# Kernel tuning notes

Hardware: AMD Instinct MI355X
Metric: run time of the kernel (lower is better)

The kernel has to match this reference:

```python
import jax, jax.numpy as jnp
import numpy as np

B, L, C, H = 4, 1024, 768, 12
D = C // H  # head_ch = 64


def setup_inputs() -> dict:
    key = jax.random.key(0)
    ks = jax.random.split(key, 8)
    s = 1.0 / np.sqrt(C)
    return {
        "inputs_q": jax.random.normal(ks[0], (B, L, C), jnp.float32),
        "inputs_kv": jax.random.normal(ks[1], (B, L, C), jnp.float32),
        "Wq": jax.random.normal(ks[2], (C, H * D), jnp.float32) * s,
        "Wk": jax.random.normal(ks[3], (C, H * D), jnp.float32) * s,
        "Wv": jax.random.normal(ks[4], (C, H * D), jnp.float32) * s,
        "Wout": jax.random.normal(ks[5], (H * D, C), jnp.float32) * s,
        "W_pre": jax.random.normal(ks[6], (H, H), jnp.float32) * (1.0 / np.sqrt(H)),
        "W_post": jax.random.normal(ks[7], (H, H), jnp.float32) * (1.0 / np.sqrt(H)),
    }


def reference(inputs_q, inputs_kv, Wq, Wk, Wv, Wout, W_pre, W_post):
    # Linear projections (no bias), split into heads: b l (h d) -> b h l d
    def split_heads(x):
        b, l, _ = x.shape
        return x.reshape(b, l, H, D).transpose(0, 2, 1, 3)

    q = split_heads(inputs_q @ Wq) / jnp.sqrt(jnp.asarray(D, inputs_q.dtype))
    k = split_heads(inputs_kv @ Wk)
    v = split_heads(inputs_kv @ Wv)

    # Attention logits [b, h, l, k]
    weights = jnp.einsum('bhld,bhkd->bhlk', q, k)
    # Talking-heads: learned cross-head mixing pre-softmax
    weights = jnp.einsum('bhlk,hi->bilk', weights, W_pre)
    weights = jax.nn.softmax(weights, axis=-1)
    # Talking-heads post-softmax mixing
    weights = jnp.einsum('bhlk,hi->bilk', weights, W_post)

    scores = jnp.einsum('bhlk,bhkd->bhld', weights, v)
    scores = scores.transpose(0, 2, 1, 3).reshape(B, L, H * D)  # b l (h d)
    return scores @ Wout
```

## Files before the change

kernel.cpp:

```cpp
#include <hip/hip_runtime.h>
#include <hip/hip_bf16.h>

#define BB 4
#define LL 1024
#define CC 768
#define HH 12
#define DD 64

typedef unsigned short ushort_t;
typedef __attribute__((ext_vector_type(8))) short bf16x8;
typedef __attribute__((ext_vector_type(4))) float f32x4;
typedef __attribute__((ext_vector_type(2))) float f32x2;
typedef __attribute__((ext_vector_type(2))) unsigned u32x2;

__device__ inline ushort_t f2bf(float x) {
    union { float f; unsigned u; } v; v.f = x;
    unsigned r = (v.u + 0x7FFFu + ((v.u >> 16) & 1u)) >> 16;
    return (ushort_t)r;
}
__device__ inline float u2f(unsigned u) {
    union { unsigned u; float f; } v; v.u = u;
    return v.f;
}
__device__ inline unsigned pack2bf(float lo, float hi) {
    union { __hip_bfloat162 v; unsigned u; } r;
    r.v = __float22bfloat162_rn(make_float2(lo, hi));
    return r.u;
}

__device__ inline void stage_rows(const ushort_t* __restrict__ g, int stride,
                                  ushort_t* lds, int nbytes, int wave, int lane) {
    const int ko = (lane & 3) << 3;
    const int rsub = lane >> 2;
    for (int off = wave * 1024; off < nbytes; off += 4096) {
        int row = (off >> 6) + rsub;
        __builtin_amdgcn_global_load_lds(
            (const __attribute__((address_space(1))) void*)(g + (size_t)row * stride + ko),
            (__attribute__((address_space(3))) void*)(lds + (off >> 1)),
            16, 0, 0);
    }
}

__global__ __launch_bounds__(256) void prep(const float* __restrict__ q, const float* __restrict__ kv,
                                            const float* __restrict__ w0, const float* __restrict__ w1,
                                            const float* __restrict__ w2, const float* __restrict__ w3,
                                            ushort_t* __restrict__ qo, ushort_t* __restrict__ kvo,
                                            ushort_t* __restrict__ o0, ushort_t* __restrict__ o1,
                                            ushort_t* __restrict__ o2, ushort_t* __restrict__ o3,
                                            float* __restrict__ Zp) {
    __shared__ float t[32][33];
    const int bx = blockIdx.x;
    if (bx < 3072) {
        const float* src = bx < 1536 ? q : kv;
        ushort_t* dst = bx < 1536 ? qo : kvo;
        int bb = bx < 1536 ? bx : bx - 1536;
        size_t i = ((size_t)bb * 256 + threadIdx.x) * 8;
        float4 a = *(const float4*)(src + i);
        float4 b = *(const float4*)(src + i + 4);
        ushort_t u[8] = {f2bf(a.x), f2bf(a.y), f2bf(a.z), f2bf(a.w),
                         f2bf(b.x), f2bf(b.y), f2bf(b.z), f2bf(b.w)};
        *(uint4*)(dst + i) = *(uint4*)u;
    } else if (bx < 5376) {
        int w = bx - 3072;
        int z = w / 576, rem = w % 576;
        const float* W = z == 0 ? w0 : z == 1 ? w1 : z == 2 ? w2 : w3;
        ushort_t* Wt   = z == 0 ? o0 : z == 1 ? o1 : z == 2 ? o2 : o3;
        const int c = threadIdx.x & 31, r0 = threadIdx.x >> 5;
        const int kb = (rem / 24) * 32, nb = (rem % 24) * 32;
#pragma unroll
        for (int i = 0; i < 4; ++i)
            t[r0 + 8 * i][c] = W[(size_t)(kb + r0 + 8 * i) * CC + nb + c];
        __syncthreads();
#pragma unroll
        for (int i = 0; i < 4; ++i)
            Wt[(size_t)(nb + r0 + 8 * i) * CC + kb + c] = f2bf(t[c][r0 + 8 * i]);
    } else {
        Zp[(bx - 5376) * 256 + threadIdx.x] = 0.f;
    }
}

__global__ __launch_bounds__(256) void proj_gemm(const ushort_t* __restrict__ Aq,
                                                 const ushort_t* __restrict__ Akv,
                                                 const ushort_t* __restrict__ Wqt,
                                                 const ushort_t* __restrict__ Wkt,
                                                 const ushort_t* __restrict__ Wvt,
                                                 ushort_t* __restrict__ Qo,
                                                 ushort_t* __restrict__ Ko,
                                                 ushort_t* __restrict__ Vto) {
    const int z = blockIdx.z;
    const ushort_t* A  = (z == 0) ? Aq : Akv;
    const ushort_t* Wt = (z == 0) ? Wqt : (z == 1 ? Wkt : Wvt);

    __shared__ __align__(16) ushort_t a_lds[128 * 32];
    __shared__ __align__(16) ushort_t b_lds[128 * 32];

    const int tid = threadIdx.x;
    const int bm = blockIdx.x * 128, bn = blockIdx.y * 128;
    const int wave = tid >> 6, lane = tid & 63;
    const int quad = lane >> 4, lq = lane & 15;
    const int wr = wave >> 1, wc = wave & 1;

    f32x4 acc[4][4] = {};

    for (int k0 = 0; k0 < CC; k0 += 32) {
        stage_rows(A + (size_t)bm * CC + k0, CC, a_lds, 8192, wave, lane);
        stage_rows(Wt + (size_t)bn * CC + k0, CC, b_lds, 8192, wave, lane);
        __syncthreads();
        bf16x8 af[4], bfr[4];
#pragma unroll
        for (int mi = 0; mi < 4; ++mi)
            af[mi] = *(bf16x8*)&a_lds[(wr * 64 + mi * 16 + lq) * 32 + quad * 8];
#pragma unroll
        for (int ni = 0; ni < 4; ++ni)
            bfr[ni] = *(bf16x8*)&b_lds[(wc * 64 + ni * 16 + lq) * 32 + quad * 8];
#pragma unroll
        for (int mi = 0; mi < 4; ++mi)
#pragma unroll
            for (int ni = 0; ni < 4; ++ni)
                acc[mi][ni] = __builtin_amdgcn_mfma_f32_16x16x32_bf16(af[mi], bfr[ni], acc[mi][ni], 0, 0, 0);
        __syncthreads();
    }

    const float scale = (z == 0) ? 0.125f : 1.0f;
#pragma unroll
    for (int mi = 0; mi < 4; ++mi)
#pragma unroll
        for (int ni = 0; ni < 4; ++ni)
#pragma unroll
            for (int r = 0; r < 4; ++r) {
                int row = bm + wr * 64 + mi * 16 + quad * 4 + r;
                int col = bn + wc * 64 + ni * 16 + lq;
                int b = row >> 10, l = row & 1023, h = col >> 6, d = col & 63;
                ushort_t v = f2bf(acc[mi][ni][r] * scale);
                if (z == 2) {
                    Vto[((size_t)(b * HH + h) * DD + d) * LL + l] = v;
                } else {
                    size_t off = (size_t)(b * HH + h) * (LL * DD)
                               + (size_t)(((l >> 4) * 8 + (d >> 3)) * 128 + (l & 15) * 8 + (d & 7));
                    if (z == 0) Qo[off] = v;
                    else        Ko[off] = v;
                }
            }
}

__global__ __launch_bounds__(256) void qk_premix(const ushort_t* __restrict__ Qf,
                                                 const ushort_t* __restrict__ Kf,
                                                 const float* __restrict__ Wpre,
                                                 ushort_t* __restrict__ E,
                                                 float* __restrict__ Z) {
    const int tid = threadIdx.x;
    const int lane = tid & 63, wave = tid >> 6;
    const int quad = lane >> 4, lq = lane & 15;
    const int wr = wave >> 1, wc = wave & 1;

    const int x = blockIdx.x;
    const int xcd = x & 7;
    const int b = xcd >> 1;
    const int s = x >> 3;
    const int bk = (s & 31) << 5;
    const int bl = ((((s >> 5) << 1) | (xcd & 1))) << 5;

    const ushort_t* Kp = Kf + (size_t)b * HH * LL * DD
                       + (size_t)(((bk >> 4) + wr) * 1024 + quad * 128 + lq * 8);
    const ushort_t* Qp = Qf + (size_t)b * HH * LL * DD
                       + (size_t)(((bl >> 4) + wc) * 1024 + quad * 128 + lq * 8);

    f32x4 acc[HH] = {};
#pragma unroll
    for (int h = 0; h < HH; ++h) {
        const size_t ho = (size_t)h * (LL * DD);
        bf16x8 ka0 = *(const bf16x8*)(Kp + ho);
        bf16x8 ka1 = *(const bf16x8*)(Kp + ho + 512);
        bf16x8 qb0 = *(const bf16x8*)(Qp + ho);
        bf16x8 qb1 = *(const bf16x8*)(Qp + ho + 512);
        acc[h] = __builtin_amdgcn_mfma_f32_16x16x32_bf16(ka0, qb0, acc[h], 0, 0, 0);
        acc[h] = __builtin_amdgcn_mfma_f32_16x16x32_bf16(ka1, qb1, acc[h], 0, 0, 0);
    }

    unsigned pk[6][4];
#pragma unroll
    for (int i2 = 0; i2 < 6; ++i2) {
        f32x4 m0 = {}, m1 = {};
#pragma unroll
        for (int h = 0; h < HH; ++h) {
            m0 += acc[h] * Wpre[h * HH + 2 * i2];
            m1 += acc[h] * Wpre[h * HH + 2 * i2 + 1];
        }
#pragma unroll
        for (int r = 0; r < 4; ++r)
            pk[i2][r] = pack2bf(__expf(m0[r]), __expf(m1[r]));
    }

    float zp[HH];
#pragma unroll
    for (int i2 = 0; i2 < 6; ++i2) {
        float s0 = 0.f, s1 = 0.f;
#pragma unroll
        for (int r = 0; r < 4; ++r) {
            s0 += u2f(pk[i2][r] << 16);
            s1 += u2f(pk[i2][r] & 0xFFFF0000u);
        }
        zp[2 * i2] = s0; zp[2 * i2 + 1] = s1;
    }
#pragma unroll
    for (int i = 0; i < HH; ++i) {
        zp[i] += __shfl_xor(zp[i], 16);
        zp[i] += __shfl_xor(zp[i], 32);
    }
    if (quad == 0) {
#pragma unroll
        for (int i = 0; i < HH; ++i)
            atomicAdd(&Z[((size_t)b * HH + i) * LL + bl + wc * 16 + lq], zp[i]);
    }

#pragma unroll
    for (int r = 0; r < 4; ++r) {
        ushort_t* ep = E + (((size_t)b * LL + bk + wr * 16 + quad * 4 + r) * LL
                            + bl + wc * 16 + lq) * HH;
        u32x2 s0; s0.x = pk[0][r]; s0.y = pk[1][r];
        u32x2 s1; s1.x = pk[2][r]; s1.y = pk[3][r];
        u32x2 s2; s2.x = pk[4][r]; s2.y = pk[5][r];
        __builtin_nontemporal_store(s0, (u32x2*)ep);
        __builtin_nontemporal_store(s1, (u32x2*)(ep + 4));
        __builtin_nontemporal_store(s2, (u32x2*)(ep + 8));
    }
}

__global__ __launch_bounds__(512) void pv_postmix(const ushort_t* __restrict__ E,
                                                  const ushort_t* __restrict__ Vt,
                                                  const float* __restrict__ Wpost,
                                                  const float* __restrict__ Z,
                                                  ushort_t* __restrict__ att) {
    __shared__ __align__(16) ushort_t p_lds[2][HH * 16 * 64];

    const int tid = threadIdx.x;
    const int lane = tid & 63, wave = tid >> 6;
    const int quad = lane >> 4, lq = lane & 15;
    const int ig = (wave >> 2) * 6;
    const int wd = wave & 3;
    const int lmix = tid & 15, kp = tid >> 4;

    const int bid = blockIdx.x;
    const int xcd = bid & 7;
    const int b = xcd >> 1;
    const int bl = ((((bid >> 3) << 1) | (xcd & 1))) << 4;

    float invZ[HH];
#pragma unroll
    for (int h = 0; h < HH; ++h)
        invZ[h] = 1.0f / Z[((size_t)b * HH + h) * LL + bl + lmix];

    const size_t vrow = ((size_t)(b * HH) * DD + wd * 16 + lq) * LL;
    const ushort_t* ebase = E + (((size_t)b * LL + kp * 2) * LL + bl + lmix) * HH;
    const size_t estep = (size_t)LL * HH;

    f32x4 acc[6] = {};
    u32x2 er[6];

#pragma unroll
    for (int j = 0; j < 3; ++j) {
        er[j]     = __builtin_nontemporal_load((const u32x2*)(ebase + 4 * j));
        er[j + 3] = __builtin_nontemporal_load((const u32x2*)(ebase + estep + 4 * j));
    }

#pragma unroll 1
    for (int kt = 0; kt < 16; ++kt) {
        unsigned w0[6] = {er[0].x, er[0].y, er[1].x, er[1].y, er[2].x, er[2].y};
        unsigned w1[6] = {er[3].x, er[3].y, er[4].x, er[4].y, er[5].x, er[5].y};
        f32x2 m[HH] = {};
#pragma unroll
        for (int h2 = 0; h2 < 6; ++h2) {
            f32x2 pe, po;
            pe.x = u2f(w0[h2] << 16);           pe.y = u2f(w1[h2] << 16);
            po.x = u2f(w0[h2] & 0xFFFF0000u);   po.y = u2f(w1[h2] & 0xFFFF0000u);
            pe *= invZ[2 * h2];
            po *= invZ[2 * h2 + 1];
#pragma unroll
            for (int i = 0; i < HH; ++i) {
                m[i] += pe * Wpost[(2 * h2) * HH + i];
                m[i] += po * Wpost[(2 * h2 + 1) * HH + i];
            }
        }

        if (kt < 15) {
            const ushort_t* ep = ebase + (size_t)(kt + 1) * 64 * estep;
#pragma unroll
            for (int j = 0; j < 3; ++j) {
                er[j]     = __builtin_nontemporal_load((const u32x2*)(ep + 4 * j));
                er[j + 3] = __builtin_nontemporal_load((const u32x2*)(ep + estep + 4 * j));
            }
        }

        {
            const int cs = (kp >> 2) ^ (lmix & 7);
            unsigned* pw = (unsigned*)p_lds[kt & 1];
#pragma unroll
            for (int i = 0; i < HH; ++i)
                pw[(i * 16 + lmix) * 32 + cs * 4 + (kp & 3)] = pack2bf(m[i].x, m[i].y);
        }

        asm volatile("s_waitcnt lgkmcnt(0)" ::: "memory");
        __builtin_amdgcn_s_barrier();
        asm volatile("" ::: "memory");

        const ushort_t* pb = p_lds[kt & 1];
#pragma unroll
        for (int k0 = 0; k0 < 2; ++k0)
#pragma unroll
            for (int ii = 0; ii < 6; ++ii) {
                const int hh = ig + ii;
                const int chl = (k0 << 2) + quad;
                const int chs = chl ^ (lq & 7);
                bf16x8 pa  = *(bf16x8*)&pb[(hh * 16 + lq) * 64 + chs * 8];
                bf16x8 vbf = *(const bf16x8*)(Vt + vrow + (size_t)hh * (DD * LL)
                                              + kt * 64 + chl * 8);
                acc[ii] = __builtin_amdgcn_mfma_f32_16x16x32_bf16(pa, vbf, acc[ii], 0, 0, 0);
            }
    }

#pragma unroll
    for (int ii = 0; ii < 6; ++ii)
#pragma unroll
        for (int r = 0; r < 4; ++r)
            att[((size_t)b * LL + bl + quad * 4 + r) * CC + (ig + ii) * 64 + wd * 16 + lq] =
                f2bf(acc[ii][r]);
}

__global__ __launch_bounds__(256) void out_gemm(const ushort_t* __restrict__ A,
                                                const ushort_t* __restrict__ Wt,
                                                float* __restrict__ out) {
    __shared__ __align__(16) ushort_t a_lds[128 * 32];
    __shared__ __align__(16) ushort_t b_lds[64 * 32];

    const int tid = threadIdx.x;
    const int bm = blockIdx.x * 128, bn = blockIdx.y * 64;
    const int wave = tid >> 6, lane = tid & 63;
    const int quad = lane >> 4, lq = lane & 15;
    const int wr = wave >> 1, wc = wave & 1;

    f32x4 acc[4][2] = {};

    for (int k0 = 0; k0 < CC; k0 += 32) {
        stage_rows(A + (size_t)bm * CC + k0, CC, a_lds, 8192, wave, lane);
        stage_rows(Wt + (size_t)bn * CC + k0, CC, b_lds, 4096, wave, lane);
        __syncthreads();
        bf16x8 af[4], bfr[2];
#pragma unroll
        for (int mi = 0; mi < 4; ++mi)
            af[mi] = *(bf16x8*)&a_lds[(wr * 64 + mi * 16 + lq) * 32 + quad * 8];
#pragma unroll
        for (int ni = 0; ni < 2; ++ni)
            bfr[ni] = *(bf16x8*)&b_lds[(wc * 32 + ni * 16 + lq) * 32 + quad * 8];
#pragma unroll
        for (int mi = 0; mi < 4; ++mi)
#pragma unroll
            for (int ni = 0; ni < 2; ++ni)
                acc[mi][ni] = __builtin_amdgcn_mfma_f32_16x16x32_bf16(af[mi], bfr[ni], acc[mi][ni], 0, 0, 0);
        __syncthreads();
    }

#pragma unroll
    for (int mi = 0; mi < 4; ++mi)
#pragma unroll
        for (int ni = 0; ni < 2; ++ni)
#pragma unroll
            for (int r = 0; r < 4; ++r) {
                int row = bm + wr * 64 + mi * 16 + quad * 4 + r;
                int col = bn + wc * 32 + ni * 16 + lq;
                out[(size_t)row * CC + col] = acc[mi][ni][r];
            }
}

extern "C" void kernel_launch(void* const* d_in, const int* in_sizes, int n_in,
                              void* d_out, int out_size, void* d_ws, size_t ws_size,
                              hipStream_t stream) {
    const float* inputs_q  = (const float*)d_in[0];
    const float* inputs_kv = (const float*)d_in[1];
    const float* Wq   = (const float*)d_in[2];
    const float* Wk   = (const float*)d_in[3];
    const float* Wv   = (const float*)d_in[4];
    const float* Wout = (const float*)d_in[5];
    const float* Wpre  = (const float*)d_in[6];
    const float* Wpost = (const float*)d_in[7];
    float* out = (float*)d_out;

    const size_t nS   = (size_t)BB * HH * LL * LL;
    const size_t nQKV = (size_t)BB * HH * LL * DD;
    const size_t nW   = (size_t)CC * CC;

    ushort_t* Eb   = (ushort_t*)d_ws;
    ushort_t* Qb   = Eb + nS;
    ushort_t* Kb   = Qb + nQKV;
    ushort_t* Vtb  = Kb + nQKV;
    ushort_t* attb = Vtb + nQKV;
    ushort_t* inq  = attb + nQKV;
    ushort_t* inkv = inq + nQKV;
    ushort_t* Wqt  = inkv + nQKV;
    ushort_t* Wkt  = Wqt + nW;
    ushort_t* Wvt  = Wkt + nW;
    ushort_t* Wot  = Wvt + nW;
    float*    Zb   = (float*)(Wot + nW);

    dim3 blk(256);

    prep<<<dim3(5568), blk, 0, stream>>>(inputs_q, inputs_kv, Wq, Wk, Wv, Wout,
                                         inq, inkv, Wqt, Wkt, Wvt, Wot, Zb);
    proj_gemm<<<dim3(32, 6, 3), blk, 0, stream>>>(inq, inkv, Wqt, Wkt, Wvt, Qb, Kb, Vtb);
    qk_premix<<<dim3(4096), blk, 0, stream>>>(Qb, Kb, Wpre, Eb, Zb);
    pv_postmix<<<dim3(256), dim3(512), 0, stream>>>(Eb, Vtb, Wpost, Zb, attb);
    out_gemm<<<dim3(32, 12), blk, 0, stream>>>(attb, Wot, out);
}
```

Baseline: 265.3 us.

## Split pv_postmix across head groups into 512 smaller blocks

The post-mix/PV kernel now launches 512 blocks of 256 threads, each handling one group of 6 output heads, instead of 256 blocks of 512 threads covering all 12 heads. Each thread post-mixes 4 key rows for only its 6 heads, which halves the LDS buffer and raises block count and occupancy. In exchange, the E tensor is read twice (once per head group) and the nontemporal loads become regular loads. V fragments are also batched into registers before the MFMA loop.

```diff
diff --git a/kernel.cpp b/kernel.cpp
--- a/kernel.cpp
+++ b/kernel.cpp
@@ -226,77 +226,93 @@
     }
 }
 
-__global__ __launch_bounds__(512) void pv_postmix(const ushort_t* __restrict__ E,
-                                                  const ushort_t* __restrict__ Vt,
-                                                  const float* __restrict__ Wpost,
-                                                  const float* __restrict__ Z,
-                                                  ushort_t* __restrict__ att) {
-    __shared__ __align__(16) ushort_t p_lds[2][HH * 16 * 64];
+__global__ __launch_bounds__(256, 3) void pv_postmix(const ushort_t* __restrict__ E,
+                                                     const ushort_t* __restrict__ Vt,
+                                                     const float* __restrict__ Wpost,
+                                                     const float* __restrict__ Z,
+                                                     ushort_t* __restrict__ att) {
+    __shared__ __align__(16) ushort_t p_lds[2][6 * 16 * 64];
 
     const int tid = threadIdx.x;
     const int lane = tid & 63, wave = tid >> 6;
     const int quad = lane >> 4, lq = lane & 15;
-    const int ig = (wave >> 2) * 6;
-    const int wd = wave & 3;
+    const int wd = wave;
     const int lmix = tid & 15, kp = tid >> 4;
 
     const int bid = blockIdx.x;
     const int xcd = bid & 7;
     const int b = xcd >> 1;
-    const int bl = ((((bid >> 3) << 1) | (xcd & 1))) << 4;
+    const int s = bid >> 3;
+    const int hg = s >> 5;
+    const int ig = hg * 6;
+    const int bl = ((((s & 31) << 1) | (xcd & 1))) << 4;
 
     float invZ[HH];
 #pragma unroll
     for (int h = 0; h < HH; ++h)
         invZ[h] = 1.0f / Z[((size_t)b * HH + h) * LL + bl + lmix];
 
-    const size_t vrow = ((size_t)(b * HH) * DD + wd * 16 + lq) * LL;
-    const ushort_t* ebase = E + (((size_t)b * LL + kp * 2) * LL + bl + lmix) * HH;
     const size_t estep = (size_t)LL * HH;
+    const ushort_t* ebase = E + (((size_t)b * LL + kp * 4) * LL + bl + lmix) * HH;
+    const size_t vbase = ((size_t)(b * HH + ig) * DD + wd * 16 + lq) * LL;
 
     f32x4 acc[6] = {};
-    u32x2 er[6];
-
-#pragma unroll
-    for (int j = 0; j < 3; ++j) {
-        er[j]     = __builtin_nontemporal_load((const u32x2*)(ebase + 4 * j));
-        er[j + 3] = __builtin_nontemporal_load((const u32x2*)(ebase + estep + 4 * j));
-    }
+    u32x2 er[12];
+
+#pragma unroll
+    for (int u = 0; u < 2; ++u)
+#pragma unroll
+        for (int j = 0; j < 3; ++j) {
+            er[u * 6 + j]     = *(const u32x2*)(ebase + (size_t)(2 * u) * estep + 4 * j);
+            er[u * 6 + 3 + j] = *(const u32x2*)(ebase + (size_t)(2 * u + 1) * estep + 4 * j);
+        }
 
 #pragma unroll 1
     for (int kt = 0; kt < 16; ++kt) {
-        unsigned w0[6] = {er[0].x, er[0].y, er[1].x, er[1].y, er[2].x, er[2].y};
-        unsigned w1[6] = {er[3].x, er[3].y, er[4].x, er[4].y, er[5].x, er[5].y};
-        f32x2 m[HH] = {};
-#pragma unroll
-        for (int h2 = 0; h2 < 6; ++h2) {
-            f32x2 pe, po;
-            pe.x = u2f(w0[h2] << 16);           pe.y = u2f(w1[h2] << 16);
-            po.x = u2f(w0[h2] & 0xFFFF0000u);   po.y = u2f(w1[h2] & 0xFFFF0000u);
-            pe *= invZ[2 * h2];
-            po *= invZ[2 * h2 + 1];
-#pragma unroll
-            for (int i = 0; i < HH; ++i) {
-                m[i] += pe * Wpost[(2 * h2) * HH + i];
-                m[i] += po * Wpost[(2 * h2 + 1) * HH + i];
+        unsigned pkw[2][6];
+#pragma unroll
+        for (int u = 0; u < 2; ++u) {
+            unsigned w0[6] = {er[u*6+0].x, er[u*6+0].y, er[u*6+1].x, er[u*6+1].y, er[u*6+2].x, er[u*6+2].y};
+            unsigned w1[6] = {er[u*6+3].x, er[u*6+3].y, er[u*6+4].x, er[u*6+4].y, er[u*6+5].x, er[u*6+5].y};
+            f32x2 m[6] = {};
+#pragma unroll
+            for (int h2 = 0; h2 < 6; ++h2) {
+                f32x2 pe, po;
+                pe.x = u2f(w0[h2] << 16);           pe.y = u2f(w1[h2] << 16);
+                po.x = u2f(w0[h2] & 0xFFFF0000u);   po.y = u2f(w1[h2] & 0xFFFF0000u);
+                pe *= invZ[2 * h2];
+                po *= invZ[2 * h2 + 1];
+#pragma unroll
+                for (int i = 0; i < 6; ++i) {
+                    m[i] += pe * Wpost[(2 * h2) * HH + ig + i];
+                    m[i] += po * Wpost[(2 * h2 + 1) * HH + ig + i];
+                }
             }
+#pragma unroll
+            for (int i = 0; i < 6; ++i) pkw[u][i] = pack2bf(m[i].x, m[i].y);
         }
 
         if (kt < 15) {
             const ushort_t* ep = ebase + (size_t)(kt + 1) * 64 * estep;
 #pragma unroll
-            for (int j = 0; j < 3; ++j) {
-                er[j]     = __builtin_nontemporal_load((const u32x2*)(ep + 4 * j));
-                er[j + 3] = __builtin_nontemporal_load((const u32x2*)(ep + estep + 4 * j));
+            for (int u = 0; u < 2; ++u)
+#pragma unroll
+                for (int j = 0; j < 3; ++j) {
+                    er[u * 6 + j]     = *(const u32x2*)(ep + (size_t)(2 * u) * estep + 4 * j);
+                    er[u * 6 + 3 + j] = *(const u32x2*)(ep + (size_t)(2 * u + 1) * estep + 4 * j);
+                }
+        }
+
+        {
+            unsigned* pw = (unsigned*)p_lds[kt & 1];
+#pragma unroll
+            for (int u = 0; u < 2; ++u) {
+                const int w = kp * 2 + u;
+                const int word = (((w >> 2) ^ (lmix & 7)) << 2) + (w & 3);
+#pragma unroll
+                for (int i = 0; i < 6; ++i)
+                    pw[(i * 16 + lmix) * 32 + word] = pkw[u][i];
             }
-        }
-
-        {
-            const int cs = (kp >> 2) ^ (lmix & 7);
-            unsigned* pw = (unsigned*)p_lds[kt & 1];
-#pragma unroll
-            for (int i = 0; i < HH; ++i)
-                pw[(i * 16 + lmix) * 32 + cs * 4 + (kp & 3)] = pack2bf(m[i].x, m[i].y);
         }
 
         asm volatile("s_waitcnt lgkmcnt(0)" ::: "memory");
@@ -305,17 +321,19 @@
 
         const ushort_t* pb = p_lds[kt & 1];
 #pragma unroll
-        for (int k0 = 0; k0 < 2; ++k0)
+        for (int k0 = 0; k0 < 2; ++k0) {
+            bf16x8 vf[6];
+#pragma unroll
+            for (int ii = 0; ii < 6; ++ii)
+                vf[ii] = *(const bf16x8*)(Vt + vbase + (size_t)ii * (DD * LL)
+                                          + kt * 64 + k0 * 32 + quad * 8);
+            const int chs = ((k0 << 2) + quad) ^ (lq & 7);
 #pragma unroll
             for (int ii = 0; ii < 6; ++ii) {
-                const int hh = ig + ii;
-                const int chl = (k0 << 2) + quad;
-                const int chs = chl ^ (lq & 7);
-                bf16x8 pa  = *(bf16x8*)&pb[(hh * 16 + lq) * 64 + chs * 8];
-                bf16x8 vbf = *(const bf16x8*)(Vt + vrow + (size_t)hh * (DD * LL)
-                                              + kt * 64 + chl * 8);
-                acc[ii] = __builtin_amdgcn_mfma_f32_16x16x32_bf16(pa, vbf, acc[ii], 0, 0, 0);
+                bf16x8 pa = *(bf16x8*)&pb[(ii * 16 + lq) * 64 + chs * 8];
+                acc[ii] = __builtin_amdgcn_mfma_f32_16x16x32_bf16(pa, vf[ii], acc[ii], 0, 0, 0);
             }
+        }
     }
 
 #pragma unroll
@@ -407,6 +425,6 @@
                                          inq, inkv, Wqt, Wkt, Wvt, Wot, Zb);
     proj_gemm<<<dim3(32, 6, 3), blk, 0, stream>>>(inq, inkv, Wqt, Wkt, Wvt, Qb, Kb, Vtb);
     qk_premix<<<dim3(4096), blk, 0, stream>>>(Qb, Kb, Wpre, Eb, Zb);
-    pv_postmix<<<dim3(256), dim3(512), 0, stream>>>(Eb, Vtb, Wpost, Zb, attb);
+    pv_postmix<<<dim3(512), blk, 0, stream>>>(Eb, Vtb, Wpost, Zb, attb);
     out_gemm<<<dim3(32, 12), blk, 0, stream>>>(attb, Wot, out);
 }
```

Measured after the change: 264.6 us. Within noise of the previous version (-0.3%).

## Tile E layout per query tile and build post-mix MFMA operands in registers

Applied to the files above, without the earlier changes.

The qk_premix kernel now writes the exp-logit tensor E in a layout blocked by 16-query tile, so each pv_postmix block reads one contiguous slice. pv_postmix drops its LDS staging and barrier. Each wave now computes the post-softmax head mixing for its own 3 output heads directly in registers, packing the results straight into MFMA A-operands, and double-buffers E loads in registers. The work per block moves from 512 to 256 threads, which means each wave recomputes the normalisation per head group, and register pressure rises considerably.

```diff
diff --git a/kernel.cpp b/kernel.cpp
--- a/kernel.cpp
+++ b/kernel.cpp
@@ -213,10 +213,11 @@
             atomicAdd(&Z[((size_t)b * HH + i) * LL + bl + wc * 16 + lq], zp[i]);
     }
 
+    const int ltw = (bl >> 4) + wc;
 #pragma unroll
     for (int r = 0; r < 4; ++r) {
-        ushort_t* ep = E + (((size_t)b * LL + bk + wr * 16 + quad * 4 + r) * LL
-                            + bl + wc * 16 + lq) * HH;
+        const int k = bk + wr * 16 + quad * 4 + r;
+        ushort_t* ep = E + (((size_t)(b * 64 + ltw) * 1024 + k) * 16 + lq) * 12;
         u32x2 s0; s0.x = pk[0][r]; s0.y = pk[1][r];
         u32x2 s1; s1.x = pk[2][r]; s1.y = pk[3][r];
         u32x2 s2; s2.x = pk[4][r]; s2.y = pk[5][r];
@@ -226,104 +227,122 @@
     }
 }
 
-__global__ __launch_bounds__(512) void pv_postmix(const ushort_t* __restrict__ E,
-                                                  const ushort_t* __restrict__ Vt,
-                                                  const float* __restrict__ Wpost,
-                                                  const float* __restrict__ Z,
-                                                  ushort_t* __restrict__ att) {
-    __shared__ __align__(16) ushort_t p_lds[2][HH * 16 * 64];
-
+__global__ __launch_bounds__(256, 1) void pv_postmix(const ushort_t* __restrict__ E,
+                                                     const ushort_t* __restrict__ Vt,
+                                                     const float* __restrict__ Wpost,
+                                                     const float* __restrict__ Z,
+                                                     ushort_t* __restrict__ att) {
     const int tid = threadIdx.x;
     const int lane = tid & 63, wave = tid >> 6;
     const int quad = lane >> 4, lq = lane & 15;
-    const int ig = (wave >> 2) * 6;
-    const int wd = wave & 3;
-    const int lmix = tid & 15, kp = tid >> 4;
+    const int hh0 = wave * 3;
 
     const int bid = blockIdx.x;
     const int xcd = bid & 7;
     const int b = xcd >> 1;
-    const int bl = ((((bid >> 3) << 1) | (xcd & 1))) << 4;
+    const int lt = ((bid >> 3) << 1) | (xcd & 1);
+    const int bl = lt << 4;
+
+    float wp[HH][3];
+#pragma unroll
+    for (int h = 0; h < HH; ++h)
+#pragma unroll
+        for (int ii = 0; ii < 3; ++ii)
+            wp[h][ii] = Wpost[h * HH + hh0 + ii];
 
     float invZ[HH];
 #pragma unroll
     for (int h = 0; h < HH; ++h)
-        invZ[h] = 1.0f / Z[((size_t)b * HH + h) * LL + bl + lmix];
-
-    const size_t vrow = ((size_t)(b * HH) * DD + wd * 16 + lq) * LL;
-    const ushort_t* ebase = E + (((size_t)b * LL + kp * 2) * LL + bl + lmix) * HH;
-    const size_t estep = (size_t)LL * HH;
-
-    f32x4 acc[6] = {};
-    u32x2 er[6];
-
-#pragma unroll
-    for (int j = 0; j < 3; ++j) {
-        er[j]     = __builtin_nontemporal_load((const u32x2*)(ebase + 4 * j));
-        er[j + 3] = __builtin_nontemporal_load((const u32x2*)(ebase + estep + 4 * j));
-    }
-
+        invZ[h] = 1.0f / Z[((size_t)b * HH + h) * LL + bl + lq];
+
+    const ushort_t* eslice = E + (size_t)(b * 64 + lt) * (1024 * 192)
+                           + (size_t)(quad * 8) * 192 + lq * 12;
+    const ushort_t* vbase = Vt + ((size_t)(b * HH + hh0) * DD + lq) * LL + quad * 8;
+
+    f32x4 acc[3][4] = {};
+    u32x2 eA[24], eB[24];
+    bf16x8 vf[12];
+
+#define LOADE(dst, kt_, k0_)                                                              \
+    do {                                                                                  \
+        const ushort_t* ep_ = eslice + (size_t)((kt_) * 64 + (k0_) * 32) * 192;           \
+        _Pragma("unroll")                                                                 \
+        for (int j_ = 0; j_ < 8; ++j_)                                                    \
+            _Pragma("unroll")                                                             \
+            for (int c_ = 0; c_ < 3; ++c_)                                                \
+                dst[j_ * 3 + c_] = *(const u32x2*)(ep_ + j_ * 192 + c_ * 4);              \
+    } while (0)
+
+#define LOADV(kt_, k0_)                                                                   \
+    do {                                                                                  \
+        _Pragma("unroll")                                                                 \
+        for (int ii_ = 0; ii_ < 3; ++ii_)                                                 \
+            _Pragma("unroll")                                                             \
+            for (int dq_ = 0; dq_ < 4; ++dq_)                                             \
+                vf[ii_ * 4 + dq_] = *(const bf16x8*)(vbase                                \
+                    + (size_t)(ii_ * DD + dq_ * 16) * LL + (kt_) * 64 + (k0_) * 32);      \
+    } while (0)
+
+#define HALF(src)                                                                         \
+    do {                                                                                  \
+        union { bf16x8 v; unsigned d[4]; } pa_[3];                                        \
+        _Pragma("unroll")                                                                 \
+        for (int j2_ = 0; j2_ < 4; ++j2_) {                                               \
+            float p0_[3] = {0.f, 0.f, 0.f}, p1_[3] = {0.f, 0.f, 0.f};                     \
+            _Pragma("unroll")                                                             \
+            for (int c_ = 0; c_ < 3; ++c_) {                                              \
+                u32x2 ea_ = src[(2 * j2_) * 3 + c_];                                      \
+                u32x2 eb_ = src[(2 * j2_ + 1) * 3 + c_];                                  \
+                float f0_ = u2f(ea_.x << 16)         * invZ[4 * c_ + 0];                  \
+                float f1_ = u2f(ea_.x & 0xFFFF0000u) * invZ[4 * c_ + 1];                  \
+                float f2_ = u2f(ea_.y << 16)         * invZ[4 * c_ + 2];                  \
+                float f3_ = u2f(ea_.y & 0xFFFF0000u) * invZ[4 * c_ + 3];                  \
+                float g0_ = u2f(eb_.x << 16)         * invZ[4 * c_ + 0];                  \
+                float g1_ = u2f(eb_.x & 0xFFFF0000u) * invZ[4 * c_ + 1];                  \
+                float g2_ = u2f(eb_.y << 16)         * invZ[4 * c_ + 2];                  \
+                float g3_ = u2f(eb_.y & 0xFFFF0000u) * invZ[4 * c_ + 3];                  \
+                _Pragma("unroll")                                                         \
+                for (int ii_ = 0; ii_ < 3; ++ii_) {                                       \
+                    p0_[ii_] += f0_ * wp[4 * c_ + 0][ii_] + f1_ * wp[4 * c_ + 1][ii_]     \
+                              + f2_ * wp[4 * c_ + 2][ii_] + f3_ * wp[4 * c_ + 3][ii_];    \
+                    p1_[ii_] += g0_ * wp[4 * c_ + 0][ii_] + g1_ * wp[4 * c_ + 1][ii_]     \
+                              + g2_ * wp[4 * c_ + 2][ii_] + g3_ * wp[4 * c_ + 3][ii_];    \
+                }                                                                         \
+            }                                                                             \
+            _Pragma("unroll")                                                             \
+            for (int ii_ = 0; ii_ < 3; ++ii_)                                             \
+                pa_[ii_].d[j2_] = pack2bf(p0_[ii_], p1_[ii_]);                            \
+        }                                                                                 \
+        _Pragma("unroll")                                                                 \
+        for (int ii_ = 0; ii_ < 3; ++ii_)                                                 \
+            _Pragma("unroll")                                                             \
+            for (int dq_ = 0; dq_ < 4; ++dq_)                                             \
+                acc[ii_][dq_] = __builtin_amdgcn_mfma_f32_16x16x32_bf16(                  \
+                    pa_[ii_].v, vf[ii_ * 4 + dq_], acc[ii_][dq_], 0, 0, 0);               \
+    } while (0)
+
+    LOADE(eA, 0, 0);
 #pragma unroll 1
     for (int kt = 0; kt < 16; ++kt) {
-        unsigned w0[6] = {er[0].x, er[0].y, er[1].x, er[1].y, er[2].x, er[2].y};
-        unsigned w1[6] = {er[3].x, er[3].y, er[4].x, er[4].y, er[5].x, er[5].y};
-        f32x2 m[HH] = {};
-#pragma unroll
-        for (int h2 = 0; h2 < 6; ++h2) {
-            f32x2 pe, po;
-            pe.x = u2f(w0[h2] << 16);           pe.y = u2f(w1[h2] << 16);
-            po.x = u2f(w0[h2] & 0xFFFF0000u);   po.y = u2f(w1[h2] & 0xFFFF0000u);
-            pe *= invZ[2 * h2];
-            po *= invZ[2 * h2 + 1];
-#pragma unroll
-            for (int i = 0; i < HH; ++i) {
-                m[i] += pe * Wpost[(2 * h2) * HH + i];
-                m[i] += po * Wpost[(2 * h2 + 1) * HH + i];
-            }
-        }
-
-        if (kt < 15) {
-            const ushort_t* ep = ebase + (size_t)(kt + 1) * 64 * estep;
-#pragma unroll
-            for (int j = 0; j < 3; ++j) {
-                er[j]     = __builtin_nontemporal_load((const u32x2*)(ep + 4 * j));
-                er[j + 3] = __builtin_nontemporal_load((const u32x2*)(ep + estep + 4 * j));
-            }
-        }
-
-        {
-            const int cs = (kp >> 2) ^ (lmix & 7);
-            unsigned* pw = (unsigned*)p_lds[kt & 1];
-#pragma unroll
-            for (int i = 0; i < HH; ++i)
-                pw[(i * 16 + lmix) * 32 + cs * 4 + (kp & 3)] = pack2bf(m[i].x, m[i].y);
-        }
-
-        asm volatile("s_waitcnt lgkmcnt(0)" ::: "memory");
-        __builtin_amdgcn_s_barrier();
-        asm volatile("" ::: "memory");
-
-        const ushort_t* pb = p_lds[kt & 1];
-#pragma unroll
-        for (int k0 = 0; k0 < 2; ++k0)
-#pragma unroll
-            for (int ii = 0; ii < 6; ++ii) {
-                const int hh = ig + ii;
-                const int chl = (k0 << 2) + quad;
-                const int chs = chl ^ (lq & 7);
-                bf16x8 pa  = *(bf16x8*)&pb[(hh * 16 + lq) * 64 + chs * 8];
-                bf16x8 vbf = *(const bf16x8*)(Vt + vrow + (size_t)hh * (DD * LL)
-                                              + kt * 64 + chl * 8);
-                acc[ii] = __builtin_amdgcn_mfma_f32_16x16x32_bf16(pa, vbf, acc[ii], 0, 0, 0);
-            }
-    }
-
-#pragma unroll
-    for (int ii = 0; ii < 6; ++ii)
-#pragma unroll
-        for (int r = 0; r < 4; ++r)
-            att[((size_t)b * LL + bl + quad * 4 + r) * CC + (ig + ii) * 64 + wd * 16 + lq] =
-                f2bf(acc[ii][r]);
+        LOADE(eB, kt, 1);
+        LOADV(kt, 0);
+        HALF(eA);
+        if (kt < 15) LOADE(eA, kt + 1, 0);
+        LOADV(kt, 1);
+        HALF(eB);
+    }
+#undef LOADE
+#undef LOADV
+#undef HALF
+
+#pragma unroll
+    for (int ii = 0; ii < 3; ++ii)
+#pragma unroll
+        for (int dq = 0; dq < 4; ++dq)
+#pragma unroll
+            for (int r = 0; r < 4; ++r)
+                att[((size_t)b * LL + bl + quad * 4 + r) * CC + (hh0 + ii) * 64 + dq * 16 + lq] =
+                    f2bf(acc[ii][dq][r]);
 }
 
 __global__ __launch_bounds__(256) void out_gemm(const ushort_t* __restrict__ A,
@@ -407,6 +426,6 @@
                                          inq, inkv, Wqt, Wkt, Wvt, Wot, Zb);
     proj_gemm<<<dim3(32, 6, 3), blk, 0, stream>>>(inq, inkv, Wqt, Wkt, Wvt, Qb, Kb, Vtb);
     qk_premix<<<dim3(4096), blk, 0, stream>>>(Qb, Kb, Wpre, Eb, Zb);
-    pv_postmix<<<dim3(256), dim3(512), 0, stream>>>(Eb, Vtb, Wpost, Zb, attb);
+    pv_postmix<<<dim3(256), blk, 0, stream>>>(Eb, Vtb, Wpost, Zb, attb);
     out_gemm<<<dim3(32, 12), blk, 0, stream>>>(attb, Wot, out);
 }
```

Result: no change. 267.2 us (+0.7%).
